# Performance work log

Hardware: AMD Instinct MI355X
Metric: run time of the kernel (lower is better)

Reference implementation:

```python
import jax, jax.numpy as jnp
import numpy as np

NUM_HEADS = 8
EPS = 1e-12  # torch F.normalize eps


def setup_inputs() -> dict:
    key = jax.random.key(0)
    k1, k2, k3 = jax.random.split(key, 3)
    b, c, h, w = 4, 384, 128, 128
    x = jax.random.normal(k1, (b, c, h, w), dtype=jnp.float32)
    qkv_w = jax.random.normal(k2, (3 * c, c), dtype=jnp.float32) * (1.0 / np.sqrt(c))
    proj_w = jax.random.normal(k3, (c, c), dtype=jnp.float32) * (1.0 / np.sqrt(c))
    temperature = jnp.ones((NUM_HEADS, 1, 1), dtype=jnp.float32)
    return {"x": x, "qkv_w": qkv_w, "proj_w": proj_w, "temperature": temperature}


def _l2_normalize(t):
    # matches torch F.normalize(dim=-1): t / max(||t||_2, eps)
    n = jnp.sqrt(jnp.sum(t * t, axis=-1, keepdims=True))
    return t / jnp.maximum(n, EPS)


def reference(x, qkv_w, proj_w, temperature):
    b, c, h, w = x.shape
    heads = NUM_HEADS
    ch = c // heads  # per-head channel dim
    n = h * w
    # 1x1 conv == channel matmul
    qkv = jnp.einsum('bchw,oc->bohw', x, qkv_w)          # [b, 3c, h, w]
    qkv = qkv.reshape(b, 3, heads, ch, n)                # split qkv / heads / flatten spatial
    q, k, v = qkv[:, 0], qkv[:, 1], qkv[:, 2]            # [b, heads, ch, n]
    q = _l2_normalize(q)
    k = _l2_normalize(k)
    attn = jnp.einsum('bhcn,bhdn->bhcd', q, k) * temperature  # [b, heads, ch, ch]
    attn = jax.nn.softmax(attn, axis=-1)
    out = jnp.einsum('bhcd,bhdn->bhcn', attn, v)         # [b, heads, ch, n]
    out = out.reshape(b, c, h, w)
    out = jnp.einsum('bchw,oc->bohw', out, proj_w)       # 1x1 projection
    return out
```

## Files before the change

### kernel.cpp

```cpp
#include <hip/hip_runtime.h>
#include <stdint.h>

#define HW 16384
#define CH 384
#define NS 16

typedef float  f32x4  __attribute__((ext_vector_type(4)));
typedef short  short8 __attribute__((ext_vector_type(8)));
typedef __bf16 bf16x8 __attribute__((ext_vector_type(8)));
typedef unsigned short u16;
typedef u16 u16x4 __attribute__((ext_vector_type(4)));

__device__ __forceinline__ u16 f2bf(float f) {
  union { float f; uint32_t u; } v; v.f = f;
  uint32_t r = v.u + 0x7fffu + ((v.u >> 16) & 1u);
  return (u16)(r >> 16);
}
__device__ __forceinline__ float bf2f(u16 v) {
  union { uint32_t u; float f; } x; x.u = ((uint32_t)v) << 16; return x.f;
}
__device__ __forceinline__ f32x4 zero4() { f32x4 z = {0.f, 0.f, 0.f, 0.f}; return z; }

__device__ __forceinline__ f32x4 mfma_bf16(short8 a, short8 b, f32x4 c) {
  return __builtin_amdgcn_mfma_f32_16x16x32_bf16(
      __builtin_bit_cast(bf16x8, a), __builtin_bit_cast(bf16x8, b), c, 0, 0, 0);
}

__device__ __forceinline__ void gload16(const void* g, void* lds) {
  auto gp = (const __attribute__((address_space(1))) uint32_t*)(uintptr_t)g;
  auto lp = (__attribute__((address_space(3))) uint32_t*)(uintptr_t)lds;
  __builtin_amdgcn_global_load_lds(gp, lp, 16, 0, 0);
}

__global__ void k_convert_w(const float* __restrict__ w, u16* __restrict__ o) {
  int i = blockIdx.x * 256 + threadIdx.x;
  if (i < 1152 * CH) o[i] = f2bf(w[i]);
}

__global__ __launch_bounds__(256) void k_wvt(const float* __restrict__ w,
                                             u16* __restrict__ wvt) {
  __shared__ u16 tl[64][72];
  const int ci = blockIdx.x, di = blockIdx.y, t = threadIdx.x;
#pragma unroll
  for (int jj = 0; jj < 4; ++jj) {
    const int r = (t >> 4) + jj * 16;
    f32x4 v = *(const f32x4*)(w + (size_t)(768 + di * 64 + r) * CH + ci * 64 + (t & 15) * 4);
#pragma unroll
    for (int i = 0; i < 4; ++i) tl[(t & 15) * 4 + i][r] = f2bf(v[i]);
  }
  __syncthreads();
#pragma unroll
  for (int jj = 0; jj < 2; ++jj) {
    const int c = (t >> 3) + jj * 32;
    short8 v = *(const short8*)(&tl[c][(t & 7) * 8]);
    *(short8*)(wvt + (size_t)(ci * 64 + c) * CH + di * 64 + (t & 7) * 8) = v;
  }
}

__global__ __launch_bounds__(256) void k_transpose_x(const float* __restrict__ x,
                                                     u16* __restrict__ xT,
                                                     u16* __restrict__ xb) {
  __shared__ u16 tile[64][72];
  const int b = blockIdx.z, c0 = blockIdx.y * 64, n0 = blockIdx.x * 64;
  const int t = threadIdx.x;
  const float* xp = x + (size_t)b * CH * HW;
  u16* xbp = xb + (size_t)b * CH * HW;
  const int nq = t & 15;
  const int cr = t >> 4;
#pragma unroll
  for (int jj = 0; jj < 4; ++jj) {
    const int c = cr + jj * 16;
    f32x4 v = *(const f32x4*)(xp + (size_t)(c0 + c) * HW + n0 + nq * 4);
    u16x4 pk;
#pragma unroll
    for (int i = 0; i < 4; ++i) { u16 bv = f2bf(v[i]); tile[nq * 4 + i][c] = bv; pk[i] = bv; }
    *(u16x4*)(xbp + (size_t)(c0 + c) * HW + n0 + nq * 4) = pk;
  }
  __syncthreads();
  u16* xtb = xT + (size_t)b * HW * CH;
  const int cc = t & 7;
  const int r0 = t >> 3;
#pragma unroll
  for (int jj = 0; jj < 2; ++jj) {
    const int r = r0 + jj * 32;
    short8 v = *(const short8*)(&tile[r][cc * 8]);
    *(short8*)(xtb + (size_t)(n0 + r) * CH + c0 + cc * 8) = v;
  }
}

__global__ __launch_bounds__(256) void k_gramx(const u16* __restrict__ xb,
                                               float* __restrict__ part) {
  const int orig = blockIdx.x;
  const int L = (orig & 7) * 48 + (orig >> 3);
  const int pair = L % 6;
  const int ns = (L / 6) % NS;
  const int b = L / (6 * NS);
  const int i = pair < 3 ? 0 : (pair < 5 ? 1 : 2);
  const int j = pair < 3 ? pair : (pair < 5 ? pair - 2 : 2);
  const int t = threadIdx.x, lane = t & 63, w = t >> 6;
  const int wo = w & 1, wn = w >> 1;
  const u16* pa = xb + ((size_t)b * CH + i * 128) * HW;
  const u16* pb = xb + ((size_t)b * CH + j * 128) * HW;

  f32x4 acc[4][4];
#pragma unroll
  for (int a = 0; a < 4; ++a)
#pragma unroll
    for (int c = 0; c < 4; ++c) acc[a][c] = zero4();

  for (int st = 0; st < 32; ++st) {
    const int n = ns * 1024 + st * 32 + ((lane >> 4) << 3);
    short8 af[4], bf[4];
#pragma unroll
    for (int mi = 0; mi < 4; ++mi)
      af[mi] = *(const short8*)(pa + (size_t)(wo * 64 + mi * 16 + (lane & 15)) * HW + n);
#pragma unroll
    for (int ni = 0; ni < 4; ++ni)
      bf[ni] = *(const short8*)(pb + (size_t)(wn * 64 + ni * 16 + (lane & 15)) * HW + n);
#pragma unroll
    for (int ni = 0; ni < 4; ++ni)
#pragma unroll
      for (int mi = 0; mi < 4; ++mi)
        acc[ni][mi] = mfma_bf16(bf[ni], af[mi], acc[ni][mi]);
  }
  float* dst = part + ((size_t)(b * 6 + pair) * NS + ns) * 16384;
#pragma unroll
  for (int ni = 0; ni < 4; ++ni)
#pragma unroll
    for (int mi = 0; mi < 4; ++mi) {
      const int ai = wo * 64 + mi * 16 + (lane & 15);
      const int bj = wn * 64 + ni * 16 + ((lane >> 4) << 2);
      *(f32x4*)(dst + (size_t)ai * 128 + bj) = acc[ni][mi];
    }
}

__global__ __launch_bounds__(256) void k_greduce(const float* __restrict__ part,
                                                 u16* __restrict__ Goff,
                                                 float* __restrict__ Gd) {
  const int cq = blockIdx.x, pair = blockIdx.y, b = blockIdx.z;
  const int i = pair < 3 ? 0 : (pair < 5 ? 1 : 2);
  const int j = pair < 3 ? pair : (pair < 5 ? pair - 2 : 2);
  const int t = threadIdx.x;
  const int c0 = cq * 32;
  __shared__ u16 tl[32][136];
  const float* src = part + (size_t)(b * 6 + pair) * NS * 16384;
#pragma unroll
  for (int p = 0; p < 4; ++p) {
    const int q = t + p * 256;
    const int ai = q >> 3;
    const int bj = c0 + (q & 7) * 4;
    f32x4 s = zero4();
    for (int ns = 0; ns < NS; ++ns) s += *(const f32x4*)(src + (size_t)ns * 16384 + ai * 128 + bj);
    if (i == j) {
#pragma unroll
      for (int jj = 0; jj < 4; ++jj)
        if (ai == bj + jj) { Gd[b * CH + i * 128 + ai] = s[jj]; s[jj] = 0.f; }
    }
    u16x4 pk;
#pragma unroll
    for (int jj = 0; jj < 4; ++jj) { pk[jj] = f2bf(s[jj]); tl[bj - c0 + jj][ai] = pk[jj]; }
    *(u16x4*)(Goff + ((size_t)b * CH + i * 128 + ai) * CH + j * 128 + bj) = pk;
  }
  if (i != j) {
    __syncthreads();
#pragma unroll
    for (int jj = 0; jj < 2; ++jj) {
      const int r = t >> 3;
      const int ch = ((t & 7) + jj * 8) * 8;
      short8 v = *(const short8*)(&tl[r][ch]);
      *(short8*)(Goff + ((size_t)b * CH + j * 128 + c0 + r) * CH + i * 128 + ch) = v;
    }
  }
}

__device__ __forceinline__ void stage32p(u16* lds, const u16* __restrict__ g, int t) {
  const int w = t >> 6;
#pragma unroll
  for (int s = 0; s < 2; ++s) {
    const int r = s * 32 + (t >> 3);
    const int g8 = (t & 7) ^ (r & 7);
    const int gr = 2 * r + (g8 >> 2);
    gload16(g + (size_t)gr * CH + (g8 & 3) * 8, lds + s * 2048 + w * 512);
  }
}

template <int TM>
__global__ __launch_bounds__(256) void k_mini(const u16* __restrict__ A,
                                              const u16* __restrict__ B,
                                              float* __restrict__ Tout,
                                              u16* __restrict__ Bout,
                                              const float* __restrict__ Gd,
                                              const u16* __restrict__ Wd) {
  const int nt = blockIdx.x, mt = blockIdx.y, b = blockIdx.z;
  __shared__ u16 Ws[4][64 * 64];
  __shared__ u16 Xs[4][64 * 64];
  const int t = threadIdx.x, lane = t & 63, w = t >> 6;
  const int wo = w & 1, wn = w >> 1;
  const u16* Ab = A + (TM ? 0 : (size_t)b * CH * CH) + (size_t)mt * 128 * CH;
  const u16* Bb = B + (TM ? (size_t)b * CH * CH : 0) + (size_t)nt * 128 * CH;

  f32x4 acc[4][4];
#pragma unroll
  for (int a = 0; a < 4; ++a)
#pragma unroll
    for (int c = 0; c < 4; ++c) acc[a][c] = zero4();

#pragma unroll
  for (int p = 0; p < 3; ++p) {
    stage32p(Ws[p], Ab + p * 32, t);
    stage32p(Xs[p], Bb + p * 32, t);
  }
  const int ks = lane >> 4;
  for (int kt = 0; kt < 12; ++kt) {
    if (kt <= 9)       asm volatile("s_waitcnt vmcnt(8)" ::: "memory");
    else if (kt == 10) asm volatile("s_waitcnt vmcnt(4)" ::: "memory");
    else               asm volatile("s_waitcnt vmcnt(0)" ::: "memory");
    asm volatile("s_barrier" ::: "memory");
    if (kt < 9) {
      stage32p(Ws[(kt + 3) & 3], Ab + (kt + 3) * 32, t);
      stage32p(Xs[(kt + 3) & 3], Bb + (kt + 3) * 32, t);
    }
    const u16* Wc = Ws[kt & 3];
    const u16* Xc = Xs[kt & 3];
    short8 af[4], bfr[4];
#pragma unroll
    for (int mi = 0; mi < 4; ++mi) {
      const int gr = wo * 64 + mi * 16 + (lane & 15);
      const int r = gr >> 1;
      const int p = ((gr & 1) * 4 + ks) ^ (r & 7);
      af[mi] = *(const short8*)(Wc + r * 64 + p * 8);
    }
#pragma unroll
    for (int ni = 0; ni < 4; ++ni) {
      const int gr = wn * 64 + ni * 16 + (lane & 15);
      const int r = gr >> 1;
      const int p = ((gr & 1) * 4 + ks) ^ (r & 7);
      bfr[ni] = *(const short8*)(Xc + r * 64 + p * 8);
    }
#pragma unroll
    for (int ni = 0; ni < 4; ++ni)
#pragma unroll
      for (int mi = 0; mi < 4; ++mi)
        acc[ni][mi] = mfma_bf16(bfr[ni], af[mi], acc[ni][mi]);
  }

#pragma unroll
  for (int ni = 0; ni < 4; ++ni)
#pragma unroll
    for (int mi = 0; mi < 4; ++mi) {
      const int tr = mt * 128 + wo * 64 + mi * 16 + (lane & 15);
      const int d0 = nt * 128 + wn * 64 + ni * 16 + ((lane >> 4) << 2);
      if (TM) {
        f32x4 g = *(const f32x4*)(Gd + b * CH + d0);
        u16x4 w4 = *(const u16x4*)(Wd + (size_t)tr * CH + d0);
        f32x4 v;
#pragma unroll
        for (int jj = 0; jj < 4; ++jj) v[jj] = acc[ni][mi][jj] + bf2f(w4[jj]) * g[jj];
        *(f32x4*)(Tout + ((size_t)b * 768 + tr) * CH + d0) = v;
      } else {
        u16x4 pk;
#pragma unroll
        for (int jj = 0; jj < 4; ++jj) pk[jj] = f2bf(acc[ni][mi][jj]);
        *(u16x4*)(Bout + ((size_t)b * CH + tr) * CH + d0) = pk;
      }
    }
}

__global__ __launch_bounds__(384) void k_attn(const float* __restrict__ T,
                                              const u16* __restrict__ wbf,
                                              const float* __restrict__ projw,
                                              const float* __restrict__ temp,
                                              u16* __restrict__ Mbf) {
  const int h = blockIdx.x, b = blockIdx.y, t = threadIdx.x;
  __shared__ float Sl[48][48];
  __shared__ float attn[48][48];
  __shared__ float nrm[96];
  const float* T1 = T + ((size_t)b * 768 + h * 48) * CH;
  const float* T2 = T1 + (size_t)384 * CH;
  const u16* wk = wbf + (size_t)(384 + h * 48) * CH;

  if (t < 64) {
    const int lane = t;
    f32x4 sa[3][3];
#pragma unroll
    for (int a = 0; a < 3; ++a)
#pragma unroll
      for (int c = 0; c < 3; ++c) sa[a][c] = zero4();
    for (int kk = 0; kk < 12; ++kk) {
      const int kc = kk * 32 + ((lane >> 4) << 3);
      short8 afr[3], bfr[3];
#pragma unroll
      for (int mi = 0; mi < 3; ++mi) {
        const float* s = T1 + (size_t)(mi * 16 + (lane & 15)) * CH + kc;
        f32x4 v0 = *(const f32x4*)(s);
        f32x4 v1 = *(const f32x4*)(s + 4);
        short8 a;
#pragma unroll
        for (int jj = 0; jj < 4; ++jj) { a[jj] = (short)f2bf(v0[jj]); a[4 + jj] = (short)f2bf(v1[jj]); }
        afr[mi] = a;
      }
#pragma unroll
      for (int ni = 0; ni < 3; ++ni)
        bfr[ni] = *(const short8*)(wk + (size_t)(ni * 16 + (lane & 15)) * CH + kc);
#pragma unroll
      for (int ni = 0; ni < 3; ++ni)
#pragma unroll
        for (int mi = 0; mi < 3; ++mi)
          sa[ni][mi] = mfma_bf16(bfr[ni], afr[mi], sa[ni][mi]);
    }
#pragma unroll
    for (int ni = 0; ni < 3; ++ni)
#pragma unroll
      for (int mi = 0; mi < 3; ++mi)
#pragma unroll
        for (int jj = 0; jj < 4; ++jj)
          Sl[mi * 16 + (lane & 15)][ni * 16 + ((lane >> 4) << 2) + jj] = sa[ni][mi][jj];
  } else if (t < 160) {
    const int r = t - 64;
    const float* Tr = (r < 48) ? T1 + (size_t)r * CH : T2 + (size_t)(r - 48) * CH;
    const u16* wr = (r < 48) ? wbf + (size_t)(h * 48 + r) * CH
                             : wbf + (size_t)(384 + h * 48 + (r - 48)) * CH;
    float a = 0.f;
    for (int c = 0; c < 384; ++c) a += Tr[c] * bf2f(wr[c]);
    nrm[r] = a;
  }
  __syncthreads();
  if (t < 48) {
    const float th = temp[h];
    const float inq = 1.f / fmaxf(sqrtf(nrm[t]), 1e-12f);
    float l[48];
    float mx = -3.4e38f;
#pragma unroll
    for (int u = 0; u < 48; ++u) {
      float ik = 1.f / fmaxf(sqrtf(nrm[48 + u]), 1e-12f);
      float lg = Sl[t][u] * inq * ik * th;
      l[u] = lg;
      mx = fmaxf(mx, lg);
    }
    float sum = 0.f;
#pragma unroll
    for (int u = 0; u < 48; ++u) { float e = __expf(l[u] - mx); l[u] = e; sum += e; }
    float inv = 1.f / sum;
#pragma unroll
    for (int u = 0; u < 48; ++u) attn[t][u] = l[u] * inv;
  }
  __syncthreads();
  float pw[48];
#pragma unroll
  for (int c = 0; c < 48; ++c) pw[c] = projw[(size_t)t * CH + h * 48 + c];
  u16* Mb = Mbf + ((size_t)b * CH + t) * CH + h * 48;
#pragma unroll 4
  for (int d = 0; d < 48; ++d) {
    float a = 0.f;
#pragma unroll
    for (int c = 0; c < 48; ++c) a = fmaf(pw[c], attn[c][d], a);
    Mb[d] = f2bf(a);
  }
}

__global__ __launch_bounds__(256) void k_final(const u16* __restrict__ P,
                                               const u16* __restrict__ Bx,
                                               float* __restrict__ outp) {
  constexpr int NWG = 3 * 128 * 4;
  constexpr int CHUNK = NWG / 8;
  const int orig = blockIdx.x;
  const int L = (orig & 7) * CHUNK + (orig >> 3);
  const int ot = L % 3;
  const int ntg = L / 3;
  const int b = ntg >> 7;
  const int nt = ntg & 127;

  __shared__ u16 Ws[4][64 * 64];
  __shared__ u16 Xs[4][64 * 64];
  const int t = threadIdx.x, lane = t & 63, w = t >> 6;
  const int wo = w & 1, wn = w >> 1;
  const u16* Ab = P + (size_t)b * CH * CH + (size_t)ot * 128 * CH;
  const u16* Bb = Bx + (size_t)b * HW * CH + (size_t)nt * 128 * CH;

  f32x4 acc[4][4];
#pragma unroll
  for (int a = 0; a < 4; ++a)
#pragma unroll
    for (int c = 0; c < 4; ++c) acc[a][c] = zero4();

#pragma unroll
  for (int p = 0; p < 3; ++p) {
    stage32p(Ws[p], Ab + p * 32, t);
    stage32p(Xs[p], Bb + p * 32, t);
  }
  const int ks = lane >> 4;
  for (int kt = 0; kt < 12; ++kt) {
    if (kt <= 9)       asm volatile("s_waitcnt vmcnt(8)" ::: "memory");
    else if (kt == 10) asm volatile("s_waitcnt vmcnt(4)" ::: "memory");
    else               asm volatile("s_waitcnt vmcnt(0)" ::: "memory");
    asm volatile("s_barrier" ::: "memory");
    if (kt < 9) {
      stage32p(Ws[(kt + 3) & 3], Ab + (kt + 3) * 32, t);
      stage32p(Xs[(kt + 3) & 3], Bb + (kt + 3) * 32, t);
    }
    const u16* Wc = Ws[kt & 3];
    const u16* Xc = Xs[kt & 3];
    short8 af[4], bfr[4];
#pragma unroll
    for (int mi = 0; mi < 4; ++mi) {
      const int gr = wo * 64 + mi * 16 + (lane & 15);
      const int r = gr >> 1;
      const int p = ((gr & 1) * 4 + ks) ^ (r & 7);
      af[mi] = *(const short8*)(Wc + r * 64 + p * 8);
    }
#pragma unroll
    for (int ni = 0; ni < 4; ++ni) {
      const int gr = wn * 64 + ni * 16 + (lane & 15);
      const int r = gr >> 1;
      const int p = ((gr & 1) * 4 + ks) ^ (r & 7);
      bfr[ni] = *(const short8*)(Xc + r * 64 + p * 8);
    }
#pragma unroll
    for (int ni = 0; ni < 4; ++ni)
#pragma unroll
      for (int mi = 0; mi < 4; ++mi)
        acc[ni][mi] = mfma_bf16(bfr[ni], af[mi], acc[ni][mi]);
  }
  float* ob = outp + (size_t)b * CH * HW;
#pragma unroll
  for (int ni = 0; ni < 4; ++ni)
#pragma unroll
    for (int mi = 0; mi < 4; ++mi) {
      int o = ot * 128 + wo * 64 + mi * 16 + (lane & 15);
      int n = nt * 128 + wn * 64 + ni * 16 + ((lane >> 4) << 2);
      *(f32x4*)(ob + (size_t)o * HW + n) = acc[ni][mi];
    }
}

extern "C" void kernel_launch(void* const* d_in, const int* in_sizes, int n_in,
                              void* d_out, int out_size, void* d_ws, size_t ws_size,
                              hipStream_t stream) {
  const float* x     = (const float*)d_in[0];
  const float* qkvw  = (const float*)d_in[1];
  const float* projw = (const float*)d_in[2];
  const float* temp  = (const float*)d_in[3];
  float* out = (float*)d_out;
  char* ws = (char*)d_ws;

  u16*   xT   = (u16*)(ws);
  u16*   wbf  = (u16*)(ws + 50331648);
  u16*   wvt  = (u16*)(ws + 51216384);
  u16*   Goff = (u16*)(ws + 51511296);
  float* Gd   = (float*)(ws + 52690944);
  float* Tf   = (float*)(ws + 52697088);
  u16*   Mbf  = (u16*)(ws + 57415680);
  u16*   Pbf  = (u16*)(ws + 58595328);
  u16*   xb   = (u16*)d_out;
  float* part = (float*)((char*)d_out + 50331648);

  k_convert_w<<<dim3((1152 * CH + 255) / 256), 256, 0, stream>>>(qkvw, wbf);
  k_wvt<<<dim3(6, 6), 256, 0, stream>>>(qkvw, wvt);
  k_transpose_x<<<dim3(HW / 64, CH / 64, 4), 256, 0, stream>>>(x, xT, xb);
  k_gramx<<<dim3(6 * NS * 4), 256, 0, stream>>>(xb, part);
  k_greduce<<<dim3(4, 6, 4), 256, 0, stream>>>(part, Goff, Gd);
  k_mini<1><<<dim3(3, 6, 4), 256, 0, stream>>>(wbf, Goff, Tf, nullptr, Gd, wbf);
  k_attn<<<dim3(8, 4), 384, 0, stream>>>(Tf, wbf, projw, temp, Mbf);
  k_mini<0><<<dim3(3, 3, 4), 256, 0, stream>>>(Mbf, wvt, nullptr, Pbf, nullptr, nullptr);
  k_final<<<dim3(3 * 128 * 4), 256, 0, stream>>>(Pbf, xT, out);
}
```

Baseline: 189.4 us.

## Stage Gram-matrix kernel through triple-buffered swizzled LDS with async loads

The x·xᵀ Gram kernel stops reading MFMA fragments directly from global memory with strided row accesses. It now stages 64x64 bf16 tiles into a 3-deep LDS ring with async global-to-LDS loads, vmcnt waits and barriers, reusing the swizzled staging helper, now templated on row stride. The spatial split doubles (NS 16 to 32), giving more blocks with shorter K loops but twice as many partial sums to reduce. A scalar norm dot product is also vectorised into 4-wide loads.

```diff
diff --git a/kernel.cpp b/kernel.cpp
--- a/kernel.cpp
+++ b/kernel.cpp
@@ -3,7 +3,7 @@
 
 #define HW 16384
 #define CH 384
-#define NS 16
+#define NS 32
 
 typedef float  f32x4  __attribute__((ext_vector_type(4)));
 typedef short  short8 __attribute__((ext_vector_type(8)));
@@ -88,10 +88,22 @@
   }
 }
 
+template <int STRIDE>
+__device__ __forceinline__ void stageS(u16* lds, const u16* __restrict__ g, int t) {
+  const int w = t >> 6;
+#pragma unroll
+  for (int s = 0; s < 2; ++s) {
+    const int r = s * 32 + (t >> 3);
+    const int g8 = (t & 7) ^ (r & 7);
+    const int gr = 2 * r + (g8 >> 2);
+    gload16(g + (size_t)gr * STRIDE + (g8 & 3) * 8, lds + s * 2048 + w * 512);
+  }
+}
+
 __global__ __launch_bounds__(256) void k_gramx(const u16* __restrict__ xb,
                                                float* __restrict__ part) {
   const int orig = blockIdx.x;
-  const int L = (orig & 7) * 48 + (orig >> 3);
+  const int L = (orig & 7) * (6 * NS * 4 / 8) + (orig >> 3);
   const int pair = L % 6;
   const int ns = (L / 6) % NS;
   const int b = L / (6 * NS);
@@ -99,8 +111,11 @@
   const int j = pair < 3 ? pair : (pair < 5 ? pair - 2 : 2);
   const int t = threadIdx.x, lane = t & 63, w = t >> 6;
   const int wo = w & 1, wn = w >> 1;
-  const u16* pa = xb + ((size_t)b * CH + i * 128) * HW;
-  const u16* pb = xb + ((size_t)b * CH + j * 128) * HW;
+  const u16* pa = xb + ((size_t)b * CH + i * 128) * HW + ns * 512;
+  const u16* pb = xb + ((size_t)b * CH + j * 128) * HW + ns * 512;
+
+  __shared__ u16 As[3][64 * 64];
+  __shared__ u16 Bs[3][64 * 64];
 
   f32x4 acc[4][4];
 #pragma unroll
@@ -108,15 +123,37 @@
 #pragma unroll
     for (int c = 0; c < 4; ++c) acc[a][c] = zero4();
 
-  for (int st = 0; st < 32; ++st) {
-    const int n = ns * 1024 + st * 32 + ((lane >> 4) << 3);
+#pragma unroll
+  for (int p = 0; p < 2; ++p) {
+    stageS<HW>(As[p], pa + p * 32, t);
+    stageS<HW>(Bs[p], pb + p * 32, t);
+  }
+  const int ks = lane >> 4;
+  for (int kt = 0; kt < 16; ++kt) {
+    if (kt < 15) asm volatile("s_waitcnt vmcnt(4)" ::: "memory");
+    else         asm volatile("s_waitcnt vmcnt(0)" ::: "memory");
+    asm volatile("s_barrier" ::: "memory");
+    if (kt <= 13) {
+      stageS<HW>(As[(kt + 2) % 3], pa + (kt + 2) * 32, t);
+      stageS<HW>(Bs[(kt + 2) % 3], pb + (kt + 2) * 32, t);
+    }
+    const u16* Ac = As[kt % 3];
+    const u16* Bc = Bs[kt % 3];
     short8 af[4], bf[4];
 #pragma unroll
-    for (int mi = 0; mi < 4; ++mi)
-      af[mi] = *(const short8*)(pa + (size_t)(wo * 64 + mi * 16 + (lane & 15)) * HW + n);
-#pragma unroll
-    for (int ni = 0; ni < 4; ++ni)
-      bf[ni] = *(const short8*)(pb + (size_t)(wn * 64 + ni * 16 + (lane & 15)) * HW + n);
+    for (int mi = 0; mi < 4; ++mi) {
+      const int gr = wo * 64 + mi * 16 + (lane & 15);
+      const int r = gr >> 1;
+      const int p = ((gr & 1) * 4 + ks) ^ (r & 7);
+      af[mi] = *(const short8*)(Ac + r * 64 + p * 8);
+    }
+#pragma unroll
+    for (int ni = 0; ni < 4; ++ni) {
+      const int gr = wn * 64 + ni * 16 + (lane & 15);
+      const int r = gr >> 1;
+      const int p = ((gr & 1) * 4 + ks) ^ (r & 7);
+      bf[ni] = *(const short8*)(Bc + r * 64 + p * 8);
+    }
 #pragma unroll
     for (int ni = 0; ni < 4; ++ni)
 #pragma unroll
@@ -170,17 +207,6 @@
       short8 v = *(const short8*)(&tl[r][ch]);
       *(short8*)(Goff + ((size_t)b * CH + j * 128 + c0 + r) * CH + i * 128 + ch) = v;
     }
-  }
-}
-
-__device__ __forceinline__ void stage32p(u16* lds, const u16* __restrict__ g, int t) {
-  const int w = t >> 6;
-#pragma unroll
-  for (int s = 0; s < 2; ++s) {
-    const int r = s * 32 + (t >> 3);
-    const int g8 = (t & 7) ^ (r & 7);
-    const int gr = 2 * r + (g8 >> 2);
-    gload16(g + (size_t)gr * CH + (g8 & 3) * 8, lds + s * 2048 + w * 512);
   }
 }
 
@@ -207,8 +233,8 @@
 
 #pragma unroll
   for (int p = 0; p < 3; ++p) {
-    stage32p(Ws[p], Ab + p * 32, t);
-    stage32p(Xs[p], Bb + p * 32, t);
+    stageS<CH>(Ws[p], Ab + p * 32, t);
+    stageS<CH>(Xs[p], Bb + p * 32, t);
   }
   const int ks = lane >> 4;
   for (int kt = 0; kt < 12; ++kt) {
@@ -217,8 +243,8 @@
     else               asm volatile("s_waitcnt vmcnt(0)" ::: "memory");
     asm volatile("s_barrier" ::: "memory");
     if (kt < 9) {
-      stage32p(Ws[(kt + 3) & 3], Ab + (kt + 3) * 32, t);
-      stage32p(Xs[(kt + 3) & 3], Bb + (kt + 3) * 32, t);
+      stageS<CH>(Ws[(kt + 3) & 3], Ab + (kt + 3) * 32, t);
+      stageS<CH>(Xs[(kt + 3) & 3], Bb + (kt + 3) * 32, t);
     }
     const u16* Wc = Ws[kt & 3];
     const u16* Xc = Xs[kt & 3];
@@ -321,7 +347,12 @@
     const u16* wr = (r < 48) ? wbf + (size_t)(h * 48 + r) * CH
                              : wbf + (size_t)(384 + h * 48 + (r - 48)) * CH;
     float a = 0.f;
-    for (int c = 0; c < 384; ++c) a += Tr[c] * bf2f(wr[c]);
+    for (int c4 = 0; c4 < 96; ++c4) {
+      f32x4 tv = *(const f32x4*)(Tr + c4 * 4);
+      u16x4 wv = *(const u16x4*)(wr + c4 * 4);
+#pragma unroll
+      for (int jj = 0; jj < 4; ++jj) a = fmaf(tv[jj], bf2f(wv[jj]), a);
+    }
     nrm[r] = a;
   }
   __syncthreads();
@@ -385,8 +416,8 @@
 
 #pragma unroll
   for (int p = 0; p < 3; ++p) {
-    stage32p(Ws[p], Ab + p * 32, t);
-    stage32p(Xs[p], Bb + p * 32, t);
+    stageS<CH>(Ws[p], Ab + p * 32, t);
+    stageS<CH>(Xs[p], Bb + p * 32, t);
   }
   const int ks = lane >> 4;
   for (int kt = 0; kt < 12; ++kt) {
@@ -395,8 +426,8 @@
     else               asm volatile("s_waitcnt vmcnt(0)" ::: "memory");
     asm volatile("s_barrier" ::: "memory");
     if (kt < 9) {
-      stage32p(Ws[(kt + 3) & 3], Ab + (kt + 3) * 32, t);
-      stage32p(Xs[(kt + 3) & 3], Bb + (kt + 3) * 32, t);
+      stageS<CH>(Ws[(kt + 3) & 3], Ab + (kt + 3) * 32, t);
+      stageS<CH>(Xs[(kt + 3) & 3], Bb + (kt + 3) * 32, t);
     }
     const u16* Wc = Ws[kt & 3];
     const u16* Xc = Xs[kt & 3];
```

New measurement: 156.5 us. -17.4%, faster.
